# Optimization experiments

Measured on AMD Instinct MI355X. Metric: run time of the kernel, lower is better.

Reference implementation:

```python
import jax, jax.numpy as jnp
import numpy as np

B, S, D_IN, D_OUT = 4, 2048, 2048, 8192


def setup_inputs() -> dict:
    key = jax.random.key(0)
    k1, k2 = jax.random.split(key)
    x = jax.random.normal(k1, (B, S, D_IN), dtype=jnp.float32)
    weight = jax.random.normal(k2, (D_OUT, D_IN), dtype=jnp.float32) * 0.02
    alpha = jnp.float32(1.0)
    bias = jnp.zeros((D_OUT,), dtype=jnp.float32)
    return {"x": x, "weight": weight, "alpha": alpha, "bias": bias}


def reference(x, weight, alpha, bias):
    # Ternary quantization: delta = 0.7 * mean(|w|); w_q in {-1,0,1} * alpha
    delta = 0.7 * jnp.mean(jnp.abs(weight))
    w_t = jnp.where(weight > delta, jnp.float32(1.0),
                    jnp.where(weight < -delta, jnp.float32(-1.0), jnp.float32(0.0)))
    w_q = w_t * alpha  # [out, in]
    # F.linear: x @ w_q^T + bias
    return jnp.einsum('bsd,od->bso', x, w_q) + bias
```

## Files before the change

### kernel.cpp

```cpp
#include <hip/hip_runtime.h>
#include <hip/hip_bf16.h>
#include <stdint.h>

typedef __attribute__((ext_vector_type(4))) int i32x4;
typedef __attribute__((ext_vector_type(16))) int i32x16;
typedef signed char s8;

#define M_TOT 8192
#define N_TOT 8192
#define K_TOT 2048
#define W_COUNT (N_TOT * K_TOT)
#define X_COUNT (M_TOT * K_TOT)

__global__ void tl_reduce(const float* __restrict__ w, const float* __restrict__ x,
                          double* __restrict__ wsum, float* __restrict__ xmax) {
    const int b = blockIdx.x;
    if (b < 1024) {
        const int tid = b * 256 + threadIdx.x;
        const float4* w4 = (const float4*)w;
        double s = 0.0;
        for (int i = tid; i < W_COUNT / 4; i += 1024 * 256) {
            float4 v = w4[i];
            s += (double)fabsf(v.x) + (double)fabsf(v.y) + (double)fabsf(v.z) + (double)fabsf(v.w);
        }
        #pragma unroll
        for (int off = 32; off > 0; off >>= 1) s += __shfl_down(s, off);
        __shared__ double red[4];
        if ((threadIdx.x & 63) == 0) red[threadIdx.x >> 6] = s;
        __syncthreads();
        if (threadIdx.x == 0) wsum[b] = (red[0] + red[1]) + (red[2] + red[3]);
    } else {
        const int tid = (b - 1024) * 256 + threadIdx.x;
        const float4* x4 = (const float4*)x;
        float m = 0.0f;
        for (int i = tid; i < X_COUNT / 4; i += 1024 * 256) {
            float4 v = x4[i];
            m = fmaxf(m, fmaxf(fmaxf(fabsf(v.x), fabsf(v.y)), fmaxf(fabsf(v.z), fabsf(v.w))));
        }
        #pragma unroll
        for (int off = 32; off > 0; off >>= 1) m = fmaxf(m, __shfl_down(m, off));
        __shared__ float redm[4];
        if ((threadIdx.x & 63) == 0) redm[threadIdx.x >> 6] = m;
        __syncthreads();
        if (threadIdx.x == 0) xmax[b - 1024] = fmaxf(fmaxf(redm[0], redm[1]), fmaxf(redm[2], redm[3]));
    }
}

__global__ void tl_finalize(const double* __restrict__ wsum, const float* __restrict__ xmax,
                            const float* __restrict__ alpha,
                            double* __restrict__ delta, float* __restrict__ qp) {
    const int t = threadIdx.x;
    double s = (wsum[t] + wsum[t + 256]) + (wsum[t + 512] + wsum[t + 768]);
    float m = fmaxf(fmaxf(xmax[t], xmax[t + 256]), fmaxf(xmax[t + 512], xmax[t + 768]));
    #pragma unroll
    for (int off = 32; off > 0; off >>= 1) {
        s += __shfl_down(s, off);
        m = fmaxf(m, __shfl_down(m, off));
    }
    __shared__ double rs[4];
    __shared__ float rm[4];
    if ((t & 63) == 0) { rs[t >> 6] = s; rm[t >> 6] = m; }
    __syncthreads();
    if (t == 0) {
        *delta = 0.7 * (((rs[0] + rs[1]) + (rs[2] + rs[3])) / (double)W_COUNT);
        float mm = fmaxf(fmaxf(rm[0], rm[1]), fmaxf(rm[2], rm[3]));
        qp[0] = 127.0f / mm;
        qp[1] = alpha[0] * (mm / 127.0f);
    }
}

__global__ void tl_tern_w(const float* __restrict__ w, const double* __restrict__ delta_p,
                          s8* __restrict__ wb) {
    const double d = *delta_p;
    const int i = (blockIdx.x * 256 + threadIdx.x) * 16;
    union { s8 c[16]; i32x4 v; } o;
    #pragma unroll
    for (int j = 0; j < 16; j += 4) {
        float4 v = *(const float4*)(w + i + j);
        float f[4] = {v.x, v.y, v.z, v.w};
        #pragma unroll
        for (int r = 0; r < 4; ++r) {
            double wd = (double)f[r];
            o.c[j + r] = wd > d ? 1 : (wd < -d ? -1 : 0);
        }
    }
    *(i32x4*)(wb + i) = o.v;
}

__global__ void tl_quant_x(const float* __restrict__ x, const float* __restrict__ qp,
                           s8* __restrict__ xb) {
    const float inv = qp[0];
    const int i = (blockIdx.x * 256 + threadIdx.x) * 16;
    union { s8 c[16]; i32x4 v; } o;
    #pragma unroll
    for (int j = 0; j < 16; j += 4) {
        float4 v = *(const float4*)(x + i + j);
        float f[4] = {v.x, v.y, v.z, v.w};
        #pragma unroll
        for (int r = 0; r < 4; ++r) {
            int q = (int)__builtin_rintf(f[r] * inv);
            q = q > 127 ? 127 : (q < -127 ? -127 : q);
            o.c[j + r] = (s8)q;
        }
    }
    *(i32x4*)(xb + i) = o.v;
}


#define SB    __builtin_amdgcn_sched_barrier(0)
#define BARR  __builtin_amdgcn_s_barrier()
#define LGKM6 asm volatile("s_waitcnt lgkmcnt(6)" ::: "memory")
#define LGKM0 asm volatile("s_waitcnt lgkmcnt(0)" ::: "memory")
#define VMW(N) asm volatile("s_waitcnt vmcnt(" #N ")" ::: "memory")
#define PRIO1 __builtin_amdgcn_s_setprio(1)
#define PRIO0 __builtin_amdgcn_s_setprio(0)

#define GLDS(SRC, DOFF) __builtin_amdgcn_global_load_lds(                      \
    (const __attribute__((address_space(1))) void*)(SRC),                      \
    (__attribute__((address_space(3))) void*)(lds + (DOFF)), 16, 0, 0)

#define RD6(AR, BR, S, KK) do {                                                \
    _Pragma("unroll") for (int m_ = 0; m_ < 4; ++m_)                           \
        AR[m_] = *(const i32x4*)(lds + (S) * 16384 + wrOff + m_ * 2048 +       \
                                 (lrd ^ ((KK) * 32)));                         \
    _Pragma("unroll") for (int n_ = 0; n_ < 2; ++n_)                           \
        BR[n_] = *(const i32x4*)(lds + 49152 + (S) * 8192 + wcOff + n_ * 2048 + \
                                 (lrd ^ ((KK) * 32)));                         \
} while (0)

#define MM(AR, BR) do {                                                        \
    _Pragma("unroll") for (int m_ = 0; m_ < 4; ++m_)                           \
    _Pragma("unroll") for (int n_ = 0; n_ < 2; ++n_)                           \
        acc[m_][n_] = __builtin_amdgcn_mfma_i32_32x32x32_i8(                   \
            AR[m_], BR[n_], acc[m_][n_], 0, 0, 0);                             \
} while (0)

#define STG_A(SS, KOFF) do {                                                   \
    _Pragma("unroll") for (int j_ = 0; j_ < 4; ++j_)                           \
        GLDS(aSrc + (size_t)(j_ * 64) * K_TOT + (KOFF),                        \
             (SS) * 16384 + j_ * 4096 + L);                                    \
} while (0)
#define STG_B(SS, KOFF) do {                                                   \
    _Pragma("unroll") for (int j_ = 0; j_ < 2; ++j_)                           \
        GLDS(bSrc + (size_t)(j_ * 64) * K_TOT + (KOFF),                        \
             49152 + (SS) * 8192 + j_ * 4096 + L);                             \
} while (0)

#define KTILE(S, SN, SG, KOFF, DOSTG, GATE, DONEXT) do {                       \
    RD6(aO, bO, S, 1);                                                         \
    SB; LGKM6; SB;                                                             \
    PRIO1; MM(aE, bE); PRIO0; SB;                                              \
    if (DOSTG) { STG_A(SG, KOFF); STG_B(SG, KOFF); }                           \
    SB; LGKM0; SB;                                                             \
    GATE; BARR; SB;                                                            \
    if (DONEXT) RD6(aE, bE, SN, 0);                                            \
    SB;                                                                        \
    PRIO1; MM(aO, bO); PRIO0; SB;                                              \
} while (0)

__global__ __launch_bounds__(256, 2) void tl_gemm_i8(
    const s8* __restrict__ A, const s8* __restrict__ Bm,
    const float* __restrict__ qp, const float* __restrict__ bias,
    float* __restrict__ C) {
    __shared__ __attribute__((aligned(128))) char lds[73728];

    const int t = threadIdx.x;
    const int wid = t >> 6;
    const int l = t & 63;
    const int wr = wid >> 1;
    const int wc = wid & 1;

    const int bid = blockIdx.x;
    const int xc = bid & 7;
    const int j = bid >> 3;
    const int tm = xc * 4 + ((j >> 4) & 3);
    const int tn = (j & 15) + (j >> 6) * 16;
    const int row0 = tm * 256, col0 = tn * 128;

    const int L = t * 16;
    const int off = L ^ (((L >> 7) & 3) << 4);
    const int sr = off >> 6;
    const int kb = off & 63;
    const s8* aSrc = A + (size_t)(row0 + sr) * K_TOT + kb;
    const s8* bSrc = Bm + (size_t)(col0 + sr) * K_TOT + kb;

    const int rl = l & 31, kg = l >> 5;
    const int lrd = rl * 64 + ((kg ^ ((rl >> 1) & 3)) << 4);
    const int wrOff = wr * 8192;
    const int wcOff = wc * 4096;

    i32x16 acc[4][2] = {};
    i32x4 aE[4], bE[2], aO[4], bO[2];

    STG_A(0, 0); STG_B(0, 0);
    STG_A(1, 64); STG_B(1, 64);
    VMW(6); BARR; SB;
    RD6(aE, bE, 0, 0);

    int koff = 128;
    #pragma unroll 1
    for (int i = 0; i < 10; ++i) {
        KTILE(0, 1, 2, koff, 1, VMW(6), 1); koff += 64;
        KTILE(1, 2, 0, koff, 1, VMW(6), 1); koff += 64;
        KTILE(2, 0, 1, koff, 1, VMW(6), 1); koff += 64;
    }
    KTILE(0, 1, 0, 0, 0, VMW(0), 1);
    KTILE(1, 0, 0, 0, 0, (void)0, 0);

    const float osc = qp[1];
    #pragma unroll
    for (int m_ = 0; m_ < 4; ++m_) {
        const int crow = row0 + wr * 128 + m_ * 32 + kg * 4;
        #pragma unroll
        for (int n_ = 0; n_ < 2; ++n_) {
            const int ccol = col0 + wc * 64 + n_ * 32 + rl;
            const float bv = bias[ccol];
            #pragma unroll
            for (int r = 0; r < 16; ++r) {
                const int row = crow + (r & 3) + 8 * (r >> 2);
                C[(size_t)row * N_TOT + ccol] = (float)acc[m_][n_][r] * osc + bv;
            }
        }
    }
}

extern "C" void kernel_launch(void* const* d_in, const int* in_sizes, int n_in,
                              void* d_out, int out_size, void* d_ws, size_t ws_size,
                              hipStream_t stream) {
    const float* x     = (const float*)d_in[0];
    const float* wgt   = (const float*)d_in[1];
    const float* alpha = (const float*)d_in[2];
    const float* bias  = (const float*)d_in[3];
    float* out = (float*)d_out;

    char* ws = (char*)d_ws;
    double* wsum = (double*)ws;
    float* xmax  = (float*)(ws + 8192);
    double* delta = (double*)(ws + 12288);
    float* qp     = (float*)(ws + 12304);
    s8* xb = (s8*)(ws + 16384);
    s8* wb = (s8*)(ws + 16384 + (size_t)X_COUNT);

    tl_reduce<<<2048, 256, 0, stream>>>(wgt, x, wsum, xmax);
    tl_finalize<<<1, 256, 0, stream>>>(wsum, xmax, alpha, delta, qp);
    tl_tern_w<<<W_COUNT / (256 * 16), 256, 0, stream>>>(wgt, delta, wb);
    tl_quant_x<<<X_COUNT / (256 * 16), 256, 0, stream>>>(x, qp, xb);
    tl_gemm_i8<<<(M_TOT / 256) * (N_TOT / 128), 256, 0, stream>>>(xb, wb, qp, bias, out);
}
```

Baseline: 207.7 us.

## Merge quantize kernels and split GEMM tile across 8 waves

Combines the weight ternarization and activation quantization kernels into a single launch that picks its branch by block index, removing one kernel launch. The int8 GEMM moves from 4 to 8 waves per block on the same 256x128 tile. Each wave now computes 64x64 with half the accumulators and fragment registers, and each thread issues fewer global-to-LDS loads, with the wait counts adjusted to match. The s_setprio hints and several sched barriers are dropped. The aim is more waves in flight to hide LDS and memory latency, at the cost of more barrier participants and less register-level reuse per wave.

```diff
diff --git a/kernel.cpp b/kernel.cpp
--- a/kernel.cpp
+++ b/kernel.cpp
@@ -69,58 +69,57 @@
     }
 }
 
-__global__ void tl_tern_w(const float* __restrict__ w, const double* __restrict__ delta_p,
-                          s8* __restrict__ wb) {
-    const double d = *delta_p;
-    const int i = (blockIdx.x * 256 + threadIdx.x) * 16;
-    union { s8 c[16]; i32x4 v; } o;
-    #pragma unroll
-    for (int j = 0; j < 16; j += 4) {
-        float4 v = *(const float4*)(w + i + j);
-        float f[4] = {v.x, v.y, v.z, v.w};
-        #pragma unroll
-        for (int r = 0; r < 4; ++r) {
-            double wd = (double)f[r];
-            o.c[j + r] = wd > d ? 1 : (wd < -d ? -1 : 0);
-        }
-    }
-    *(i32x4*)(wb + i) = o.v;
-}
-
-__global__ void tl_quant_x(const float* __restrict__ x, const float* __restrict__ qp,
-                           s8* __restrict__ xb) {
-    const float inv = qp[0];
-    const int i = (blockIdx.x * 256 + threadIdx.x) * 16;
-    union { s8 c[16]; i32x4 v; } o;
-    #pragma unroll
-    for (int j = 0; j < 16; j += 4) {
-        float4 v = *(const float4*)(x + i + j);
-        float f[4] = {v.x, v.y, v.z, v.w};
-        #pragma unroll
-        for (int r = 0; r < 4; ++r) {
-            int q = (int)__builtin_rintf(f[r] * inv);
-            q = q > 127 ? 127 : (q < -127 ? -127 : q);
-            o.c[j + r] = (s8)q;
-        }
-    }
-    *(i32x4*)(xb + i) = o.v;
+__global__ void tl_quant(const float* __restrict__ w, const float* __restrict__ x,
+                         const double* __restrict__ delta_p, const float* __restrict__ qp,
+                         s8* __restrict__ wb, s8* __restrict__ xb) {
+    const int b = blockIdx.x;
+    if (b < 4096) {
+        const double d = *delta_p;
+        const int i = (b * 256 + threadIdx.x) * 16;
+        union { s8 c[16]; i32x4 v; } o;
+        #pragma unroll
+        for (int j = 0; j < 16; j += 4) {
+            float4 v = *(const float4*)(w + i + j);
+            float f[4] = {v.x, v.y, v.z, v.w};
+            #pragma unroll
+            for (int r = 0; r < 4; ++r) {
+                double wd = (double)f[r];
+                o.c[j + r] = wd > d ? 1 : (wd < -d ? -1 : 0);
+            }
+        }
+        *(i32x4*)(wb + i) = o.v;
+    } else {
+        const float inv = qp[0];
+        const int i = ((b - 4096) * 256 + threadIdx.x) * 16;
+        union { s8 c[16]; i32x4 v; } o;
+        #pragma unroll
+        for (int j = 0; j < 16; j += 4) {
+            float4 v = *(const float4*)(x + i + j);
+            float f[4] = {v.x, v.y, v.z, v.w};
+            #pragma unroll
+            for (int r = 0; r < 4; ++r) {
+                int q = (int)__builtin_rintf(f[r] * inv);
+                q = q > 127 ? 127 : (q < -127 ? -127 : q);
+                o.c[j + r] = (s8)q;
+            }
+        }
+        *(i32x4*)(xb + i) = o.v;
+    }
 }
 
 
 #define SB    __builtin_amdgcn_sched_barrier(0)
 #define BARR  __builtin_amdgcn_s_barrier()
-#define LGKM6 asm volatile("s_waitcnt lgkmcnt(6)" ::: "memory")
+#define LGKM4 asm volatile("s_waitcnt lgkmcnt(4)" ::: "memory")
 #define LGKM0 asm volatile("s_waitcnt lgkmcnt(0)" ::: "memory")
 #define VMW(N) asm volatile("s_waitcnt vmcnt(" #N ")" ::: "memory")
-#define PRIO1 __builtin_amdgcn_s_setprio(1)
-#define PRIO0 __builtin_amdgcn_s_setprio(0)
 
 #define GLDS(SRC, DOFF) __builtin_amdgcn_global_load_lds(                      \
     (const __attribute__((address_space(1))) void*)(SRC),                      \
     (__attribute__((address_space(3))) void*)(lds + (DOFF)), 16, 0, 0)
 
-#define RD6(AR, BR, S, KK) do {                                                \
-    _Pragma("unroll") for (int m_ = 0; m_ < 4; ++m_)                           \
+#define RD4(AR, BR, S, KK) do {                                                \
+    _Pragma("unroll") for (int m_ = 0; m_ < 2; ++m_)                           \
         AR[m_] = *(const i32x4*)(lds + (S) * 16384 + wrOff + m_ * 2048 +       \
                                  (lrd ^ ((KK) * 32)));                         \
     _Pragma("unroll") for (int n_ = 0; n_ < 2; ++n_)                           \
@@ -128,37 +127,33 @@
                                  (lrd ^ ((KK) * 32)));                         \
 } while (0)
 
-#define MM(AR, BR) do {                                                        \
-    _Pragma("unroll") for (int m_ = 0; m_ < 4; ++m_)                           \
+#define MM4(AR, BR) do {                                                       \
+    _Pragma("unroll") for (int m_ = 0; m_ < 2; ++m_)                           \
     _Pragma("unroll") for (int n_ = 0; n_ < 2; ++n_)                           \
         acc[m_][n_] = __builtin_amdgcn_mfma_i32_32x32x32_i8(                   \
             AR[m_], BR[n_], acc[m_][n_], 0, 0, 0);                             \
 } while (0)
 
 #define STG_A(SS, KOFF) do {                                                   \
-    _Pragma("unroll") for (int j_ = 0; j_ < 4; ++j_)                           \
-        GLDS(aSrc + (size_t)(j_ * 64) * K_TOT + (KOFF),                        \
-             (SS) * 16384 + j_ * 4096 + L);                                    \
-} while (0)
-#define STG_B(SS, KOFF) do {                                                   \
-    _Pragma("unroll") for (int j_ = 0; j_ < 2; ++j_)                           \
-        GLDS(bSrc + (size_t)(j_ * 64) * K_TOT + (KOFF),                        \
-             49152 + (SS) * 8192 + j_ * 4096 + L);                             \
-} while (0)
+    GLDS(aSrc + (KOFF), (SS) * 16384 + L);                                     \
+    GLDS(aSrc + (KOFF) + (size_t)128 * K_TOT, (SS) * 16384 + 8192 + L);        \
+} while (0)
+#define STG_B(SS, KOFF)                                                        \
+    GLDS(bSrc + (KOFF), 49152 + (SS) * 8192 + L)
 
 #define KTILE(S, SN, SG, KOFF, DOSTG, GATE, DONEXT) do {                       \
-    RD6(aO, bO, S, 1);                                                         \
-    SB; LGKM6; SB;                                                             \
-    PRIO1; MM(aE, bE); PRIO0; SB;                                              \
+    RD4(aO, bO, S, 1);                                                         \
+    LGKM4; SB;                                                                 \
+    MM4(aE, bE);                                                               \
     if (DOSTG) { STG_A(SG, KOFF); STG_B(SG, KOFF); }                           \
-    SB; LGKM0; SB;                                                             \
-    GATE; BARR; SB;                                                            \
-    if (DONEXT) RD6(aE, bE, SN, 0);                                            \
-    SB;                                                                        \
-    PRIO1; MM(aO, bO); PRIO0; SB;                                              \
-} while (0)
-
-__global__ __launch_bounds__(256, 2) void tl_gemm_i8(
+    LGKM0; SB;                                                                 \
+    GATE; SB;                                                                  \
+    BARR;                                                                      \
+    if (DONEXT) RD4(aE, bE, SN, 0);                                            \
+    MM4(aO, bO);                                                               \
+} while (0)
+
+__global__ __launch_bounds__(512, 4) void tl_gemm_i8(
     const s8* __restrict__ A, const s8* __restrict__ Bm,
     const float* __restrict__ qp, const float* __restrict__ bias,
     float* __restrict__ C) {
@@ -186,31 +181,31 @@
 
     const int rl = l & 31, kg = l >> 5;
     const int lrd = rl * 64 + ((kg ^ ((rl >> 1) & 3)) << 4);
-    const int wrOff = wr * 8192;
+    const int wrOff = wr * 4096;
     const int wcOff = wc * 4096;
 
-    i32x16 acc[4][2] = {};
-    i32x4 aE[4], bE[2], aO[4], bO[2];
+    i32x16 acc[2][2] = {};
+    i32x4 aE[2], bE[2], aO[2], bO[2];
 
     STG_A(0, 0); STG_B(0, 0);
     STG_A(1, 64); STG_B(1, 64);
-    VMW(6); BARR; SB;
-    RD6(aE, bE, 0, 0);
+    VMW(3); SB; BARR;
+    RD4(aE, bE, 0, 0);
 
     int koff = 128;
     #pragma unroll 1
     for (int i = 0; i < 10; ++i) {
-        KTILE(0, 1, 2, koff, 1, VMW(6), 1); koff += 64;
-        KTILE(1, 2, 0, koff, 1, VMW(6), 1); koff += 64;
-        KTILE(2, 0, 1, koff, 1, VMW(6), 1); koff += 64;
+        KTILE(0, 1, 2, koff, 1, VMW(3), 1); koff += 64;
+        KTILE(1, 2, 0, koff, 1, VMW(3), 1); koff += 64;
+        KTILE(2, 0, 1, koff, 1, VMW(3), 1); koff += 64;
     }
     KTILE(0, 1, 0, 0, 0, VMW(0), 1);
     KTILE(1, 0, 0, 0, 0, (void)0, 0);
 
     const float osc = qp[1];
     #pragma unroll
-    for (int m_ = 0; m_ < 4; ++m_) {
-        const int crow = row0 + wr * 128 + m_ * 32 + kg * 4;
+    for (int m_ = 0; m_ < 2; ++m_) {
+        const int crow = row0 + wr * 64 + m_ * 32 + kg * 4;
         #pragma unroll
         for (int n_ = 0; n_ < 2; ++n_) {
             const int ccol = col0 + wc * 64 + n_ * 32 + rl;
@@ -243,7 +238,6 @@
 
     tl_reduce<<<2048, 256, 0, stream>>>(wgt, x, wsum, xmax);
     tl_finalize<<<1, 256, 0, stream>>>(wsum, xmax, alpha, delta, qp);
-    tl_tern_w<<<W_COUNT / (256 * 16), 256, 0, stream>>>(wgt, delta, wb);
-    tl_quant_x<<<X_COUNT / (256 * 16), 256, 0, stream>>>(x, qp, xb);
-    tl_gemm_i8<<<(M_TOT / 256) * (N_TOT / 128), 256, 0, stream>>>(xb, wb, qp, bias, out);
-}
+    tl_quant<<<8192, 256, 0, stream>>>(wgt, x, delta, qp, wb, xb);
+    tl_gemm_i8<<<(M_TOT / 256) * (N_TOT / 128), 512, 0, stream>>>(xb, wb, qp, bias, out);
+}
```

Result: no change. 206.8 us, median of 2 (-0.4%).
